# Performance work log

Hardware: AMD Instinct MI355X
Metric: run time of the kernel (lower is better)

Reference implementation:

```python
import jax, jax.numpy as jnp
import numpy as np
from jax import lax

GS, NB, NC = 7, 2, 20
CONF_THR = 0.2
IOU_THR = 0.5
IMG_W = IMG_H = 448.0


def _conv(x, w, b, stride=1):
    y = lax.conv_general_dilated(x, w, (stride, stride), ((1, 1), (1, 1)),
                                 dimension_numbers=('NCHW', 'OIHW', 'NCHW'))
    return y + b[None, :, None, None]


def _lrelu(x):
    return jnp.where(x >= 0, x, 0.1 * x)


def _head(features, w1, b1, w2, b2, w3, b3, w4, b4, fc1_w, fc1_b, fc2_w, fc2_b):
    x = _lrelu(_conv(features, w1, b1))            # [B,1024,14,14]
    x = _lrelu(_conv(x, w2, b2, stride=2))         # [B,1024,7,7]
    x = _lrelu(_conv(x, w3, b3))
    x = _lrelu(_conv(x, w4, b4))
    x = x.reshape(x.shape[0], -1)                  # NCHW flatten, matches torch .view
    x = _lrelu(x @ fc1_w + fc1_b)
    x = jax.nn.sigmoid(x @ fc2_w + fc2_b)
    return x.reshape(-1, GS, GS, 5 * NB + NC)      # [B, j, i, 30]


def _decode(out):
    # replicate loop order: i outer, j inner, k inner-most; outputs indexed [b, j, i, :]
    B = out.shape[0]
    cell = 1.0 / GS
    o = jnp.swapaxes(out, 1, 2)                    # [b, i, j, c]
    bx = o[..., :5 * NB].reshape(B, GS, GS, NB, 5)
    scores = bx[..., 4]                            # [B,i,j,k]
    idx = jnp.arange(GS, dtype=out.dtype)
    x0 = idx[None, :, None, None] * cell           # uses i
    y0 = idx[None, None, :, None] * cell           # uses j
    cx = bx[..., 0] * cell + x0
    cy = bx[..., 1] * cell + y0
    w, h = bx[..., 2], bx[..., 3]
    boxes = jnp.stack([cx - 0.5 * w, cy - 0.5 * h, cx + 0.5 * w, cy + 0.5 * h], -1)
    labels = o[..., 5 * NB:].reshape(B, GS * GS, NC)   # one label vec per cell, (i,j) order
    return boxes.reshape(B, -1, 4), scores.reshape(B, -1), labels


def _nms_keep(boxes, scores, valid):
    # greedy NMS over N=GS*GS*NB candidates; invalid candidates sorted last
    N = scores.shape[0]
    s = jnp.where(valid, scores, -1.0)
    order = jnp.argsort(-s)
    b = boxes[order]
    v = valid[order]
    x1, y1, x2, y2 = b[:, 0], b[:, 1], b[:, 2], b[:, 3]
    areas = (x2 - x1) * (y2 - y1)
    iw = jnp.clip(jnp.minimum(x2[:, None], x2[None, :]) - jnp.maximum(x1[:, None], x1[None, :]), 0)
    ih = jnp.clip(jnp.minimum(y2[:, None], y2[None, :]) - jnp.maximum(y1[:, None], y1[None, :]), 0)
    inter = iw * ih
    iou = inter / (areas[:, None] + areas[None, :] - inter)
    later = jnp.arange(N)

    def body(i, state):
        suppressed, keep = state
        ki = v[i] & ~suppressed[i]
        suppressed = jnp.where(ki, suppressed | ((iou[i] > IOU_THR) & (later > i)), suppressed)
        keep = keep.at[i].set(ki)
        return suppressed, keep

    _, keep = lax.fori_loop(0, N, body, (jnp.zeros(N, bool), jnp.zeros(N, bool)))
    return jnp.zeros(N, bool).at[order].set(keep)


def setup_inputs() -> dict:
    key = jax.random.key(0)
    ks = jax.random.split(key, 8)
    B = 16
    d = {
        'features': jax.random.normal(ks[0], (B, 2048, 14, 14), jnp.float32),
        'w1': jax.random.normal(ks[1], (1024, 2048, 3, 3), jnp.float32) * 0.01,
        'b1': jnp.zeros((1024,), jnp.float32),
        'w2': jax.random.normal(ks[2], (1024, 1024, 3, 3), jnp.float32) * 0.01,
        'b2': jnp.zeros((1024,), jnp.float32),
        'w3': jax.random.normal(ks[3], (1024, 1024, 3, 3), jnp.float32) * 0.01,
        'b3': jnp.zeros((1024,), jnp.float32),
        'w4': jax.random.normal(ks[4], (1024, 1024, 3, 3), jnp.float32) * 0.01,
        'b4': jnp.zeros((1024,), jnp.float32),
        'fc1_w': jax.random.normal(ks[5], (50176, 4096), jnp.float32) * 0.004,
        'fc1_b': jnp.zeros((4096,), jnp.float32),
        'fc2_w': jax.random.normal(ks[6], (4096, GS * GS * (5 * NB + NC)), jnp.float32) * 0.02,
        'fc2_b': jnp.zeros((GS * GS * (5 * NB + NC),), jnp.float32),
    }
    return d


def reference(features, w1, b1, w2, b2, w3, b3, w4, b4, fc1_w, fc1_b, fc2_w, fc2_b):
    out = _head(features, w1, b1, w2, b2, w3, b3, w4, b4, fc1_w, fc1_b, fc2_w, fc2_b)
    boxes, scores, labels = _decode(out)           # [B,98,4],[B,98],[B,49,20]
    valid = scores >= CONF_THR                     # 'if proba < 0.2: continue' with proba=score*1.0
    keep = jax.vmap(_nms_keep)(boxes, scores, valid)  # [B,98] bool
    boxes_px = jnp.where(keep[..., None], boxes * IMG_W, 0.0)
    scores_k = jnp.where(keep, scores, 0.0)
    return boxes_px, scores_k, keep, labels
```

## Files before the change

### kernel.cpp

```cpp
#include <hip/hip_runtime.h>
#include <cstddef>

#define CONF_THR 0.2f
#define IOU_THR  0.5f
#define IMG_SZ   448.0f

typedef __attribute__((ext_vector_type(8))) _Float16 half8;
typedef __attribute__((ext_vector_type(4))) float f32x4;
typedef unsigned short u16;
typedef unsigned int   u32;

__device__ __forceinline__ u16 f2h(float x) {
    _Float16 h = (_Float16)x;
    return __builtin_bit_cast(u16, h);
}
__device__ __forceinline__ float h2f(u16 b) {
    _Float16 h = __builtin_bit_cast(_Float16, b);
    return (float)h;
}

#define GLOAD_LDS16(gsrc, ldst)                                              \
    __builtin_amdgcn_global_load_lds(                                        \
        (const __attribute__((address_space(1))) void*)(gsrc),               \
        (__attribute__((address_space(3))) void*)(ldst), 16, 0, 0)

__global__ __launch_bounds__(256)
void pad_split(const float* __restrict__ x, u16* __restrict__ xp,
               const int Cin, const int H, const int W,
               const int PW, const int PHW, const long PS)
{
    __shared__ float lds[64][200];
    const int t  = threadIdx.x;
    const int b  = blockIdx.x >> 5;
    const int cc = blockIdx.x & 31;
    const int ci0 = cc * 64;
    const int HW = H * W;

    for (int r = 0; r < 64; ++r) {
        for (int i = t; i < HW; i += 256)
            lds[r][i] = x[((long)b * Cin + ci0 + r) * HW + i];
    }
    __syncthreads();

    const int lci = t & 63;
    const int lp  = t >> 6;
    for (int pp = 0; pp < PHW / 4; ++pp) {
        const int pix = pp * 4 + lp;
        const int py = pix / PW, px = pix % PW;
        float v = 0.f;
        if (py >= 1 && py <= H && px >= 1 && px <= W)
            v = lds[lci][(py - 1) * W + (px - 1)];
        v *= 16.0f;
        u16 h = f2h(v);
        u16 m = f2h(v - h2f(h));
        const long off = ((long)b * PHW + pix) * Cin + ci0 + lci;
        xp[off] = h; xp[PS + off] = m;
    }
}

__global__ __launch_bounds__(256)
void wsplit_kernel(const float* __restrict__ w, u16* __restrict__ wT, int Cin)
{
    __shared__ float ws_l[2304];
    const int t  = threadIdx.x;
    const int cb = blockIdx.x;
    const int co = blockIdx.y;
    const long base = ((long)co * Cin + cb * 256) * 9;
    for (int i = t; i < 2304; i += 256) ws_l[i] = w[base + i];
    __syncthreads();
    const int ci = cb * 256 + t;
    const long PS = (long)9 * 1024 * Cin;
    #pragma unroll
    for (int tap = 0; tap < 9; ++tap) {
        float v = ws_l[t * 9 + tap] * 256.0f;
        u16 h = f2h(v);
        u16 m = f2h(v - h2f(h));
        long off = ((long)tap * 1024 + co) * Cin + ci;
        wT[off] = h; wT[PS + off] = m;
    }
}

template<int STRIDE>
__global__ __launch_bounds__(512, 4)
void conv_mfma(const u16* __restrict__ xp, const u16* __restrict__ wT,
               float* __restrict__ partial,
               const int Cin, const int PW, const int PHW,
               const int Wout, const int Ntot,
               const int sppsh, const int steps_pb, const int Npad,
               const long PSx)
{
    __shared__ u16 Alds[256 * 64];
    __shared__ u16 Blds[128 * 64];

    const int t  = threadIdx.x;
    const int m0 = blockIdx.x * 256;
    const int n0 = blockIdx.y * 128;
    const int g0 = blockIdx.z * steps_pb;
    const int HWout = Wout * Wout;

    int bpix[2], bblk[2];
    #pragma unroll
    for (int c = 0; c < 2; ++c) {
        const int idx = c * 512 + t;
        const int col = idx >> 3;
        const int blk = idx & 7;
        int n = n0 + col; if (n >= Ntot) n = 0;
        const int b  = n / HWout;
        const int rp = n - b * HWout;
        const int oy = rp / Wout;
        const int ox = rp - oy * Wout;
        bpix[c] = b * PHW + oy * STRIDE * PW + ox * STRIDE;
        bblk[c] = (blk ^ (col & 7)) * 8;
    }
    const int arow = t >> 3;
    const int ablk = ((t & 7) ^ (arow & 7)) * 8;
    const int wbase = (t & 448) * 16;

    const int wid = t >> 6, l = t & 63;
    const int wm = wid >> 1, wn = wid & 1;
    const int l16 = l & 15, lhi = l >> 4;

    const f32x4 zero4 = {0.f, 0.f, 0.f, 0.f};
    f32x4 acc[4][4];
    #pragma unroll
    for (int i = 0; i < 4; ++i)
        #pragma unroll
        for (int j = 0; j < 4; ++j) acc[i][j] = zero4;

    for (int s = 0; s < steps_pb; ++s) {
        const int g     = g0 + s;
        const int phase = g >> sppsh;
        const int cs    = g - (phase << sppsh);
        const int pair  = phase / 9;
        const int tap   = phase - pair * 9;
        const int pA = (0x100 >> (pair * 4)) & 15;
        const int pB = (0x010 >> (pair * 4)) & 15;
        const int ci0 = cs * 64;
        const int tapoff = (tap / 3) * PW + (tap % 3);

        const u16* Ag = wT + ((long)(pA * 9 + tap) * 1024 + m0) * Cin + ci0 + ablk;
        #pragma unroll
        for (int c = 0; c < 4; ++c)
            GLOAD_LDS16(Ag + (long)(c * 64 + arow) * Cin,
                        (char*)Alds + c * 8192 + wbase);
        const u16* Bg = xp + (long)pB * PSx + (long)tapoff * Cin + ci0;
        #pragma unroll
        for (int c = 0; c < 2; ++c)
            GLOAD_LDS16(Bg + (long)bpix[c] * Cin + bblk[c],
                        (char*)Blds + c * 8192 + wbase);

        __syncthreads();

        #pragma unroll
        for (int j = 0; j < 2; ++j) {
            const int kb = j * 64 + lhi * 16;
            half8 af[4], bf[4];
            #pragma unroll
            for (int f = 0; f < 4; ++f) {
                const int row = wm * 64 + f * 16 + l16;
                af[f] = *(const half8*)((const char*)Alds + row * 128
                                        + (kb ^ ((row & 7) << 4)));
            }
            #pragma unroll
            for (int f = 0; f < 4; ++f) {
                const int cc = wn * 64 + f * 16 + l16;
                bf[f] = *(const half8*)((const char*)Blds + cc * 128
                                        + (kb ^ ((cc & 7) << 4)));
            }
            #pragma unroll
            for (int fm = 0; fm < 4; ++fm)
                #pragma unroll
                for (int fn = 0; fn < 4; ++fn)
                    acc[fm][fn] = __builtin_amdgcn_mfma_f32_16x16x32_f16(
                        af[fm], bf[fn], acc[fm][fn], 0, 0, 0);
        }
        __syncthreads();
    }

    const long pbase = (long)blockIdx.z * 1024;
    #pragma unroll
    for (int fm = 0; fm < 4; ++fm) {
        #pragma unroll
        for (int r = 0; r < 4; ++r) {
            const long mrow = pbase + m0 + wm * 64 + fm * 16 + lhi * 4 + r;
            float* prow = partial + mrow * Npad + n0 + wn * 64 + l16;
            #pragma unroll
            for (int fn = 0; fn < 4; ++fn)
                prow[fn * 16] = acc[fm][fn][r];
        }
    }
}

__global__ __launch_bounds__(256)
void reduce_nhwc(const float* __restrict__ partial, const float* __restrict__ bias,
                 u16* __restrict__ yp,
                 const int S, const int Npad, const int Ntot,
                 const int Wout, const int PW, const int PHW, const long PSy)
{
    __shared__ float lds[64][65];
    const int t  = threadIdx.x;
    const int m0 = blockIdx.x * 64;
    const int n0 = blockIdx.y * 64;
    const int HWout = Wout * Wout;

    const int lm = t >> 6, ln = t & 63;
    for (int r = 0; r < 16; ++r) {
        const int m = r * 4 + lm;
        const int n = n0 + ln;
        float v = 0.f;
        if (n < Ntot) {
            for (int s = 0; s < S; ++s)
                v += partial[((long)s * 1024 + m0 + m) * Npad + n];
            v = v * (1.0f / 4096.0f) + bias[m0 + m];
            v = (v >= 0.f) ? v : 0.1f * v;
        }
        lds[m][ln] = v;
    }
    __syncthreads();

    const int wn_ = t >> 6, wci = t & 63;
    for (int r = 0; r < 16; ++r) {
        const int pr = r * 4 + wn_;
        const int nn = n0 + pr;
        if (nn < Ntot) {
            const int b = nn / HWout;
            const int p = nn - b * HWout;
            const int py = p / Wout + 1, px = p % Wout + 1;
            const long off = ((long)b * PHW + py * PW + px) * 1024 + m0 + wci;
            const float vs = lds[wci][pr] * 16.0f;
            u16 h = f2h(vs);
            u16 m = f2h(vs - h2f(h));
            yp[off] = h; yp[PSy + off] = m;
        }
    }
}

__global__ __launch_bounds__(256)
void reduce_f32(const float* __restrict__ partial, const float* __restrict__ bias,
                float* __restrict__ yf,
                const int S, const int Npad, const int Ntot, const int HWout)
{
    const long idx = (long)blockIdx.x * 256 + threadIdx.x;
    if (idx >= (long)1024 * Ntot) return;
    const int m = (int)(idx / Ntot);
    const int n = (int)(idx - (long)m * Ntot);
    float v = 0.f;
    for (int s = 0; s < S; ++s)
        v += partial[((long)s * 1024 + m) * Npad + n];
    v = v * (1.0f / 4096.0f) + bias[m];
    v = (v >= 0.f) ? v : 0.1f * v;
    const int b = n / HWout, pix = n - b * HWout;
    yf[((long)b * 1024 + m) * HWout + pix] = v;
}

__global__ __launch_bounds__(256)
void fc1_partial(const float* __restrict__ x, const float* __restrict__ w,
                 float* __restrict__ part)
{
    __shared__ float xs[512][16];
    const int tid = threadIdx.x;
    const int n   = blockIdx.x * 1024 + tid * 4;
    const int kc  = blockIdx.y;
    const int k0  = kc * 512;

    for (int i = tid; i < 512 * 16; i += 256) {
        const int j = i >> 4;
        const int b = i & 15;
        xs[j][b] = x[(size_t)b * 50176 + k0 + j];
    }
    __syncthreads();

    f32x4 acc[16];
    #pragma unroll
    for (int b = 0; b < 16; ++b) acc[b] = (f32x4){0.f, 0.f, 0.f, 0.f};

    for (int j = 0; j < 512; ++j) {
        const f32x4 wv = *(const f32x4*)&w[(size_t)(k0 + j) * 4096 + n];
        #pragma unroll
        for (int b = 0; b < 16; ++b) {
            const float xb = xs[j][b];
            #pragma unroll
            for (int c = 0; c < 4; ++c)
                acc[b][c] = fmaf(xb, wv[c], acc[b][c]);
        }
    }

    #pragma unroll
    for (int b = 0; b < 16; ++b)
        *(f32x4*)&part[((size_t)kc * 16 + b) * 4096 + n] = acc[b];
}

__global__ __launch_bounds__(256)
void fc1_reduce(const float* __restrict__ part, const float* __restrict__ bias,
                float* __restrict__ y)
{
    const int i = blockIdx.x * 256 + threadIdx.x;
    float s = 0.f;
    for (int kc = 0; kc < 98; ++kc) s += part[(size_t)kc * 65536 + i];
    s += bias[i & 4095];
    y[i] = (s >= 0.f) ? s : 0.1f * s;
}

__global__ __launch_bounds__(256)
void fc2_partial(const float* __restrict__ x, const float* __restrict__ w,
                 float* __restrict__ part)
{
    __shared__ float xs[128][16];
    const int tid = threadIdx.x;
    const int n   = blockIdx.x * 256 + tid;
    const int kc  = blockIdx.y;
    const int k0  = kc * 128;

    for (int i = tid; i < 128 * 16; i += 256) {
        const int j = i >> 4;
        const int b = i & 15;
        xs[j][b] = x[(size_t)b * 4096 + k0 + j];
    }
    __syncthreads();

    float acc[16] = {};
    if (n < 1470) {
        for (int j = 0; j < 128; ++j) {
            const float wv = w[(size_t)(k0 + j) * 1470 + n];
            #pragma unroll
            for (int b4 = 0; b4 < 4; ++b4) {
                const float4 xv = *(const float4*)&xs[j][b4 * 4];
                acc[b4*4+0] = fmaf(xv.x, wv, acc[b4*4+0]);
                acc[b4*4+1] = fmaf(xv.y, wv, acc[b4*4+1]);
                acc[b4*4+2] = fmaf(xv.z, wv, acc[b4*4+2]);
                acc[b4*4+3] = fmaf(xv.w, wv, acc[b4*4+3]);
            }
        }
        #pragma unroll
        for (int b = 0; b < 16; ++b)
            part[((size_t)kc * 16 + b) * 1470 + n] = acc[b];
    }
}

__global__ __launch_bounds__(256)
void fc2_reduce(const float* __restrict__ part, const float* __restrict__ bias,
                float* __restrict__ y)
{
    const int i = blockIdx.x * 256 + threadIdx.x;
    if (i >= 16 * 1470) return;
    float s = 0.f;
    for (int kc = 0; kc < 32; ++kc) s += part[(size_t)kc * 23520 + i];
    const int n = i % 1470;
    s += bias[n];
    y[i] = 1.0f / (1.0f + expf(-s));
}

__global__ __launch_bounds__(128)
void decode_nms(const float* __restrict__ out2, float* __restrict__ dout)
{
    const int b = blockIdx.x;
    const int t = threadIdx.x;
    const float cell = 1.0f / 7.0f;
    const float* o = out2 + (size_t)b * 1470;

    __shared__ float bx[98][4];
    __shared__ float sc[98];
    __shared__ float area[98];
    __shared__ int   order[98];
    __shared__ int   rankof[98];
    __shared__ int   supp[98];
    __shared__ int   keep_s[98];

    if (t < 98) {
        const int gA = t / 14;
        const int r  = t % 14;
        const int gB = r >> 1;
        const int nb = r & 1;
        const int base = gB * 210 + gA * 30 + nb * 5;
        const float v0 = o[base + 0];
        const float v1 = o[base + 1];
        const float w  = o[base + 2];
        const float h  = o[base + 3];
        const float s  = o[base + 4];
        const float cx = v0 * cell + (float)gA * cell;
        const float cy = v1 * cell + (float)gB * cell;
        const float x1 = cx - 0.5f * w;
        const float y1 = cy - 0.5f * h;
        const float x2 = cx + 0.5f * w;
        const float y2 = cy + 0.5f * h;
        bx[t][0] = x1; bx[t][1] = y1; bx[t][2] = x2; bx[t][3] = y2;
        sc[t] = s;
        area[t] = (x2 - x1) * (y2 - y1);
        supp[t] = 0;
        keep_s[t] = 0;
    }
    __syncthreads();

    if (t < 98) {
        const float si = (sc[t] >= CONF_THR) ? sc[t] : -1.0f;
        int rank = 0;
        for (int j = 0; j < 98; ++j) {
            const float sj = (sc[j] >= CONF_THR) ? sc[j] : -1.0f;
            rank += (sj > si) || (sj == si && j < t);
        }
        order[rank] = t;
        rankof[t] = rank;
    }
    __syncthreads();

    for (int i = 0; i < 98; ++i) {
        const int oi = order[i];
        const bool ki = (sc[oi] >= CONF_THR) && (supp[i] == 0);
        if (t == 0) keep_s[i] = ki ? 1 : 0;
        if (ki && t < 98 && t > i) {
            const int oj = order[t];
            const float xx1 = fmaxf(bx[oi][0], bx[oj][0]);
            const float yy1 = fmaxf(bx[oi][1], bx[oj][1]);
            const float xx2 = fminf(bx[oi][2], bx[oj][2]);
            const float yy2 = fminf(bx[oi][3], bx[oj][3]);
            const float iw = fmaxf(xx2 - xx1, 0.f);
            const float ih = fmaxf(yy2 - yy1, 0.f);
            const float inter = iw * ih;
            const float iou = inter / (area[oi] + area[oj] - inter);
            if (iou > IOU_THR) supp[t] = 1;
        }
        __syncthreads();
    }

    float* out_boxes  = dout;
    float* out_scores = dout + 6272;
    float* out_keep   = dout + 7840;
    float* out_labels = dout + 9408;

    if (t < 98) {
        const bool kp = keep_s[rankof[t]] != 0;
        const size_t bi = ((size_t)b * 98 + t) * 4;
        out_boxes[bi + 0] = kp ? bx[t][0] * IMG_SZ : 0.f;
        out_boxes[bi + 1] = kp ? bx[t][1] * IMG_SZ : 0.f;
        out_boxes[bi + 2] = kp ? bx[t][2] * IMG_SZ : 0.f;
        out_boxes[bi + 3] = kp ? bx[t][3] * IMG_SZ : 0.f;
        out_scores[(size_t)b * 98 + t] = kp ? sc[t] : 0.f;
        out_keep[(size_t)b * 98 + t]   = kp ? 1.f : 0.f;
    }
    for (int i = t; i < 49 * 20; i += 128) {
        const int g  = i / 20;
        const int c  = i - g * 20;
        const int gA = g / 7;
        const int gB = g - gA * 7;
        out_labels[(size_t)b * 980 + i] = o[gB * 210 + gA * 30 + 10 + c];
    }
}

extern "C" void kernel_launch(void* const* d_in, const int* in_sizes, int n_in,
                              void* d_out, int out_size, void* d_ws, size_t ws_size,
                              hipStream_t stream)
{
    (void)in_sizes; (void)n_in; (void)out_size; (void)ws_size;

    const float* features = (const float*)d_in[0];
    const float* w1 = (const float*)d_in[1];
    const float* b1 = (const float*)d_in[2];
    const float* w2 = (const float*)d_in[3];
    const float* b2 = (const float*)d_in[4];
    const float* w3 = (const float*)d_in[5];
    const float* b3 = (const float*)d_in[6];
    const float* w4 = (const float*)d_in[7];
    const float* b4 = (const float*)d_in[8];
    const float* fc1_w = (const float*)d_in[9];
    const float* fc1_b = (const float*)d_in[10];
    const float* fc2_w = (const float*)d_in[11];
    const float* fc2_b = (const float*)d_in[12];

    char* W = (char*)d_ws;
    size_t o = 0;
    auto alloc = [&](size_t bytes) -> char* {
        char* r = W + o; o += (bytes + 255) & ~(size_t)255; return r;
    };
    u16*   wT      = (u16*)  alloc(75497472ULL);
    u16*   xp      = (u16*)  alloc(33554432ULL);
    u16*   actA    = (u16*)  alloc(16777216ULL);
    float* a4      = (float*)alloc(3211264ULL);
    float* partial = (float*)alloc(58720256ULL);
    float* fc1o    = (float*)alloc(262144ULL);
    float* part2   = (float*)alloc(3010560ULL);
    float* fc2o    = (float*)alloc(94080ULL);
    (void)alloc(4096);
    float* part1 = (float*)xp;
    u16*   actB  = (u16*)(xp + (24u << 20) / 2);

    const long PSxp = 8388608L;
    const long PSa  = 4194304L;
    const long PSb  = 1327104L;

    pad_split<<<512, 256, 0, stream>>>(features, xp, 2048, 14, 14, 16, 256, PSxp);

    wsplit_kernel<<<dim3(8, 1024), 256, 0, stream>>>(w1, wT, 2048);
    hipMemsetAsync(actA, 0, 16777216ULL, stream);
    conv_mfma<1><<<dim3(4, 25, 4), 512, 0, stream>>>(
        xp, wT, partial, 2048, 16, 256, 14, 3136, 5, 216, 3200, PSxp);
    hipMemsetAsync(actB, 0, 5308416ULL, stream);
    reduce_nhwc<<<dim3(16, 49), 256, 0, stream>>>(partial, b1, actA,
                                                  4, 3200, 3136, 14, 16, 256, PSa);

    wsplit_kernel<<<dim3(4, 1024), 256, 0, stream>>>(w2, wT, 1024);
    conv_mfma<2><<<dim3(4, 7, 16), 512, 0, stream>>>(
        actA, wT, partial, 1024, 16, 256, 7, 784, 4, 27, 896, PSa);
    reduce_nhwc<<<dim3(16, 13), 256, 0, stream>>>(partial, b2, actB,
                                                  16, 896, 784, 7, 9, 81, PSb);

    wsplit_kernel<<<dim3(4, 1024), 256, 0, stream>>>(w3, wT, 1024);
    conv_mfma<1><<<dim3(4, 7, 16), 512, 0, stream>>>(
        actB, wT, partial, 1024, 9, 81, 7, 784, 4, 27, 896, PSb);
    reduce_nhwc<<<dim3(16, 13), 256, 0, stream>>>(partial, b3, actB,
                                                  16, 896, 784, 7, 9, 81, PSb);

    wsplit_kernel<<<dim3(4, 1024), 256, 0, stream>>>(w4, wT, 1024);
    conv_mfma<1><<<dim3(4, 7, 16), 512, 0, stream>>>(
        actB, wT, partial, 1024, 9, 81, 7, 784, 4, 27, 896, PSb);
    reduce_f32<<<3136, 256, 0, stream>>>(partial, b4, a4, 16, 896, 784, 49);

    fc1_partial<<<dim3(4, 98), 256, 0, stream>>>(a4, fc1_w, part1);
    fc1_reduce<<<256, 256, 0, stream>>>(part1, fc1_b, fc1o);

    fc2_partial<<<dim3(6, 32), 256, 0, stream>>>(fc1o, fc2_w, part2);
    fc2_reduce<<<92, 256, 0, stream>>>(part2, fc2_b, fc2o);

    decode_nms<<<16, 128, 0, stream>>>(fc2o, (float*)d_out);
}
```

Baseline: 1.131 ms.

## Fuse weight splits into one launch and raise split-K parallelism

Replaces four separate weight-split launches with one kernel that converts all four conv weight tensors into separate buffers up front. It also raises the split-K factor of every conv (8 slices for layer 1, 27 for layers 2-4), so more blocks are in flight, and bumps the occupancy hint in launch bounds. The cost is a larger partial-sum buffer, more reduction traffic, extra workspace for the separate weight buffers, and possible register pressure from the tighter launch bound.

```diff
diff --git a/kernel.cpp b/kernel.cpp
--- a/kernel.cpp
+++ b/kernel.cpp
@@ -59,11 +59,21 @@
 }
 
 __global__ __launch_bounds__(256)
-void wsplit_kernel(const float* __restrict__ w, u16* __restrict__ wT, int Cin)
+void wsplit_all(const float* __restrict__ w1, const float* __restrict__ w2,
+                const float* __restrict__ w3, const float* __restrict__ w4,
+                u16* __restrict__ wT1, u16* __restrict__ wT2,
+                u16* __restrict__ wT3, u16* __restrict__ wT4)
 {
     __shared__ float ws_l[2304];
-    const int t  = threadIdx.x;
-    const int cb = blockIdx.x;
+    const int t = threadIdx.x;
+    const int z = blockIdx.z;
+    int layer, cb;
+    if (z < 2) { layer = 0; cb = z * 4 + blockIdx.x; }
+    else       { layer = z - 1; cb = blockIdx.x; }
+    const float* w = (layer == 0) ? w1 : (layer == 1) ? w2 : (layer == 2) ? w3 : w4;
+    u16* wT        = (layer == 0) ? wT1 : (layer == 1) ? wT2 : (layer == 2) ? wT3 : wT4;
+    const int Cin  = (layer == 0) ? 2048 : 1024;
+
     const int co = blockIdx.y;
     const long base = ((long)co * Cin + cb * 256) * 9;
     for (int i = t; i < 2304; i += 256) ws_l[i] = w[base + i];
@@ -81,7 +91,7 @@
 }
 
 template<int STRIDE>
-__global__ __launch_bounds__(512, 4)
+__global__ __launch_bounds__(512, 6)
 void conv_mfma(const u16* __restrict__ xp, const u16* __restrict__ wT,
                float* __restrict__ partial,
                const int Cin, const int PW, const int PHW,
@@ -471,11 +481,14 @@
     auto alloc = [&](size_t bytes) -> char* {
         char* r = W + o; o += (bytes + 255) & ~(size_t)255; return r;
     };
-    u16*   wT      = (u16*)  alloc(75497472ULL);
+    u16*   wT1     = (u16*)  alloc(75497472ULL);
+    u16*   wT2     = (u16*)  alloc(37748736ULL);
+    u16*   wT3     = (u16*)  alloc(37748736ULL);
+    u16*   wT4     = (u16*)  alloc(37748736ULL);
     u16*   xp      = (u16*)  alloc(33554432ULL);
     u16*   actA    = (u16*)  alloc(16777216ULL);
     float* a4      = (float*)alloc(3211264ULL);
-    float* partial = (float*)alloc(58720256ULL);
+    float* partial = (float*)alloc(104857600ULL);
     float* fc1o    = (float*)alloc(262144ULL);
     float* part2   = (float*)alloc(3010560ULL);
     float* fc2o    = (float*)alloc(94080ULL);
@@ -488,31 +501,29 @@
     const long PSb  = 1327104L;
 
     pad_split<<<512, 256, 0, stream>>>(features, xp, 2048, 14, 14, 16, 256, PSxp);
-
-    wsplit_kernel<<<dim3(8, 1024), 256, 0, stream>>>(w1, wT, 2048);
+    wsplit_all<<<dim3(4, 1024, 5), 256, 0, stream>>>(w1, w2, w3, w4,
+                                                     wT1, wT2, wT3, wT4);
+
     hipMemsetAsync(actA, 0, 16777216ULL, stream);
-    conv_mfma<1><<<dim3(4, 25, 4), 512, 0, stream>>>(
-        xp, wT, partial, 2048, 16, 256, 14, 3136, 5, 216, 3200, PSxp);
+    conv_mfma<1><<<dim3(4, 25, 8), 512, 0, stream>>>(
+        xp, wT1, partial, 2048, 16, 256, 14, 3136, 5, 108, 3200, PSxp);
     hipMemsetAsync(actB, 0, 5308416ULL, stream);
     reduce_nhwc<<<dim3(16, 49), 256, 0, stream>>>(partial, b1, actA,
-                                                  4, 3200, 3136, 14, 16, 256, PSa);
-
-    wsplit_kernel<<<dim3(4, 1024), 256, 0, stream>>>(w2, wT, 1024);
-    conv_mfma<2><<<dim3(4, 7, 16), 512, 0, stream>>>(
-        actA, wT, partial, 1024, 16, 256, 7, 784, 4, 27, 896, PSa);
+                                                  8, 3200, 3136, 14, 16, 256, PSa);
+
+    conv_mfma<2><<<dim3(4, 7, 27), 512, 0, stream>>>(
+        actA, wT2, partial, 1024, 16, 256, 7, 784, 4, 16, 896, PSa);
     reduce_nhwc<<<dim3(16, 13), 256, 0, stream>>>(partial, b2, actB,
-                                                  16, 896, 784, 7, 9, 81, PSb);
-
-    wsplit_kernel<<<dim3(4, 1024), 256, 0, stream>>>(w3, wT, 1024);
-    conv_mfma<1><<<dim3(4, 7, 16), 512, 0, stream>>>(
-        actB, wT, partial, 1024, 9, 81, 7, 784, 4, 27, 896, PSb);
+                                                  27, 896, 784, 7, 9, 81, PSb);
+
+    conv_mfma<1><<<dim3(4, 7, 27), 512, 0, stream>>>(
+        actB, wT3, partial, 1024, 9, 81, 7, 784, 4, 16, 896, PSb);
     reduce_nhwc<<<dim3(16, 13), 256, 0, stream>>>(partial, b3, actB,
-                                                  16, 896, 784, 7, 9, 81, PSb);
-
-    wsplit_kernel<<<dim3(4, 1024), 256, 0, stream>>>(w4, wT, 1024);
-    conv_mfma<1><<<dim3(4, 7, 16), 512, 0, stream>>>(
-        actB, wT, partial, 1024, 9, 81, 7, 784, 4, 27, 896, PSb);
-    reduce_f32<<<3136, 256, 0, stream>>>(partial, b4, a4, 16, 896, 784, 49);
+                                                  27, 896, 784, 7, 9, 81, PSb);
+
+    conv_mfma<1><<<dim3(4, 7, 27), 512, 0, stream>>>(
+        actB, wT4, partial, 1024, 9, 81, 7, 784, 4, 16, 896, PSb);
+    reduce_f32<<<3136, 256, 0, stream>>>(partial, b4, a4, 27, 896, 784, 49);
 
     fc1_partial<<<dim3(4, 98), 256, 0, stream>>>(a4, fc1_w, part1);
     fc1_reduce<<<256, 256, 0, stream>>>(part1, fc1_b, fc1o);
```

Result: slower. 3.639 ms (+221.8%).
